# Performance work log

Measured on AMD Instinct MI355X. Metric: run time of the kernel, lower is better.

## Reference

```python
import jax, jax.numpy as jnp
import numpy as np

H = 8          # num_heads
DIM = 1024     # embed dim
DH = DIM // H // 2   # per-branch head dim = 64
B, N = 2, 2048
LAMBDA_INIT = 0.5
COS_MIN, COS_MAX = 0.0, 15.0
ALPHA = 0.5            # cos_head_residual_alpha
COS_EPS = 1e-6
RMS_EPS = 1e-5
# raw init so that sigmoid(raw) = (cos_scale_init - min)/(max - min) = 1/15
RAW_INIT = float(np.log((1.0/15.0) / (1.0 - 1.0/15.0)))


def setup_inputs() -> dict:
    key = jax.random.key(0)
    ks = jax.random.split(key, 10)
    s = 1.0 / np.sqrt(DIM)
    return {
        "x": jax.random.normal(ks[0], (B, N, DIM), jnp.float32),
        "Wq": jax.random.normal(ks[1], (DIM, DIM), jnp.float32) * s,
        "Wk": jax.random.normal(ks[2], (DIM, DIM), jnp.float32) * s,
        "Wv": jax.random.normal(ks[3], (DIM, DIM), jnp.float32) * s,
        "Wo": jax.random.normal(ks[4], (DIM, DIM), jnp.float32) * s,
        "bo": jnp.zeros((DIM,), jnp.float32),
        "lambda_q1": jax.random.normal(ks[5], (DH,), jnp.float32) * 0.1,
        "lambda_k1": jax.random.normal(ks[6], (DH,), jnp.float32) * 0.1,
        "lambda_q2": jax.random.normal(ks[7], (DH,), jnp.float32) * 0.1,
        "lambda_k2": jax.random.normal(ks[8], (DH,), jnp.float32) * 0.1,
        "delta_gain": jax.random.normal(ks[9], (H,), jnp.float32) * 0.1,
        "cos_head_delta": jnp.zeros((H,), jnp.float32),
        "cos_logit_scale_raw": jnp.float32(RAW_INIT),
        "subln_weight": jnp.ones((2 * DH,), jnp.float32),
    }


def _l2norm(t):
    # F.normalize: x / max(||x||_2, eps)
    return t / jnp.maximum(jnp.linalg.norm(t, axis=-1, keepdims=True), COS_EPS)


def reference(x, Wq, Wk, Wv, Wo, bo,
              lambda_q1, lambda_k1, lambda_q2, lambda_k2,
              delta_gain, cos_head_delta, cos_logit_scale_raw, subln_weight):
    b, n, c = x.shape
    # projections (torch Linear: x @ W.T)
    q = (x @ Wq.T).reshape(b, n, H, 2, DH).transpose(0, 2, 3, 1, 4)  # (B,H,2,N,Dh)
    k = (x @ Wk.T).reshape(b, n, H, 2, DH).transpose(0, 2, 3, 1, 4)
    v = (x @ Wv.T).reshape(b, n, H, 2 * DH).transpose(0, 2, 1, 3)    # (B,H,N,2Dh)
    q1, q2 = q[:, :, 0], q[:, :, 1]
    k1, k2 = k[:, :, 0], k[:, :, 1]

    # smooth-bounded cosine logit scale with per-head residual
    gscale = COS_MIN + (COS_MAX - COS_MIN) * jax.nn.sigmoid(cos_logit_scale_raw)
    head_delta = cos_head_delta - cos_head_delta.mean()
    cos_scale = (gscale * (1.0 + ALPHA * jnp.tanh(head_delta))).reshape(1, H, 1, 1)

    L1 = jnp.einsum('bhnd,bhmd->bhnm', _l2norm(q1), _l2norm(k1)) * cos_scale
    L2 = jnp.einsum('bhnd,bhmd->bhnm', _l2norm(q2), _l2norm(k2)) * cos_scale
    L1 = jnp.nan_to_num(L1)
    L2 = jnp.nan_to_num(L2)

    # tanh-gated interaction between branches
    G = jnp.tanh(delta_gain.reshape(1, H, 1, 1) * (L1 - L2))
    A1 = jax.nn.softmax((L1 + G).astype(jnp.float32), axis=-1).astype(x.dtype)
    A2 = jax.nn.softmax((L2 - G).astype(jnp.float32), axis=-1).astype(x.dtype)

    lambda_1 = jnp.exp(jnp.sum(lambda_q1 * lambda_k1))
    lambda_2 = jnp.exp(jnp.sum(lambda_q2 * lambda_k2))
    lambda_full = (lambda_1 - lambda_2 + LAMBDA_INIT).astype(x.dtype)

    attn = A1 - lambda_full * A2
    y = jnp.einsum('bhnm,bhmd->bhnd', attn, v)  # (B,H,N,2Dh)

    # sub-layer RMSNorm over last dim (2*Dh) with affine weight
    y = y * jax.lax.rsqrt(jnp.mean(y * y, axis=-1, keepdims=True) + RMS_EPS) * subln_weight
    y = y * (1.0 - LAMBDA_INIT)

    y = y.transpose(0, 2, 1, 3).reshape(b, n, c)
    return y @ Wo.T + bo
```

## Files before the change

kernel.cpp:

```cpp
#include <hip/hip_runtime.h>
#include <hip/hip_bf16.h>
#include <cstdint>

typedef __attribute__((ext_vector_type(8))) short short8_t;
typedef __attribute__((ext_vector_type(4))) float f32x4;
typedef __attribute__((ext_vector_type(16))) float f32x16;

#define LOG2E 1.4426950408889634f

__device__ __forceinline__ ushort f2bf(float f){
  union { float f; uint32_t i; } x; x.f = f;
  uint32_t r = x.i + 0x7FFFu + ((x.i >> 16) & 1u);
  return (ushort)(r >> 16);
}
__device__ __forceinline__ float fexp2(float x){
  float r; asm("v_exp_f32 %0, %1" : "=v"(r) : "v"(x)); return r;
}
__device__ __forceinline__ uint32_t cvtpk_bf16(float lo, float hi){
  uint32_t r;
  asm("v_cvt_pk_bf16_f32 %0, %1, %2" : "=v"(r) : "v"(lo), "v"(hi));
  return r;
}
__device__ __forceinline__ void pl32swap(uint32_t &a, uint32_t &b){
  asm volatile("v_permlane32_swap_b32 %0, %1" : "+v"(a), "+v"(b));
}
union PF { uint32_t u[4]; short8_t v; };

__global__ __launch_bounds__(256) void cvt_all_kernel(const float* __restrict__ x,
                                                      const float* __restrict__ Wq,
                                                      const float* __restrict__ Wk,
                                                      const float* __restrict__ Wv,
                                                      const float* __restrict__ Wo,
                                                      ushort* __restrict__ xb,
                                                      ushort* __restrict__ wqb,
                                                      ushort* __restrict__ wkb,
                                                      ushort* __restrict__ wvb,
                                                      ushort* __restrict__ wob){
  int bid = blockIdx.x;
  const float* s; ushort* d; int i;
  if (bid < 4096){ s = x; d = xb; i = bid * 256 + threadIdx.x; }
  else {
    int sel = (bid - 4096) >> 10;
    s = sel == 0 ? Wq : sel == 1 ? Wk : sel == 2 ? Wv : Wo;
    d = sel == 0 ? wqb : sel == 1 ? wkb : sel == 2 ? wvb : wob;
    i = ((bid - 4096) & 1023) * 256 + threadIdx.x;
  }
  float4 v = ((const float4*)s)[i];
  ushort4 o;
  o.x = f2bf(v.x); o.y = f2bf(v.y); o.z = f2bf(v.z); o.w = f2bf(v.w);
  ((ushort4*)d)[i] = o;
}

__global__ void prep_kernel(const float* __restrict__ lq1, const float* __restrict__ lk1,
                            const float* __restrict__ lq2, const float* __restrict__ lk2,
                            const float* __restrict__ dgain, const float* __restrict__ chd,
                            const float* __restrict__ rawp, float* __restrict__ sc){
  int lane = threadIdx.x;
  float p1 = lq1[lane] * lk1[lane];
  float p2 = lq2[lane] * lk2[lane];
  #pragma unroll
  for (int o = 1; o < 64; o <<= 1){
    p1 += __shfl_xor(p1, o, 64);
    p2 += __shfl_xor(p2, o, 64);
  }
  if (lane == 0) sc[24] = expf(p1) - expf(p2) + 0.5f;
  if (lane < 8){
    float m = 0.f;
    for (int i = 0; i < 8; i++) m += chd[i];
    m *= 0.125f;
    float gs = 15.f / (1.f + expf(-rawp[0]));
    float cs = gs * (1.f + 0.5f * tanhf(chd[lane] - m));
    sc[lane]      = LOG2E * cs;
    sc[8 + lane]  = LOG2E * (cs + 1.f);
    sc[16 + lane] = 2.f * dgain[lane];
  }
}

__global__ __launch_bounds__(256) void gemm_qkv(const ushort* __restrict__ A,
                                                const ushort* __restrict__ wqb,
                                                const ushort* __restrict__ wkb,
                                                const ushort* __restrict__ wvb,
                                                ushort* __restrict__ Qs,
                                                ushort* __restrict__ Kn,
                                                ushort* __restrict__ Vt,
                                                const float* __restrict__ sc){
  constexpr int N = 1024, K = 1024;
  __shared__ ushort As[128*32];
  __shared__ ushort Bs[128*32];
  const int z = blockIdx.z;
  const ushort* Bm = z == 0 ? wqb : (z == 1 ? wkb : wvb);
  const int t = threadIdx.x;
  const int lane = t & 63;
  const int w = t >> 6;
  const int wr = w >> 1, wc = w & 1;
  const long Ar0 = (long)blockIdx.x * 128;
  const long Br0 = (long)blockIdx.y * 128;
  const int r15 = lane & 15;
  const int kb = (lane >> 4) * 8;

  f32x4 acc[4][4];
  #pragma unroll
  for (int m = 0; m < 4; m++)
    #pragma unroll
    for (int n = 0; n < 4; n++) acc[m][n] = (f32x4){0.f, 0.f, 0.f, 0.f};

  for (int k0 = 0; k0 < K; k0 += 32){
    __syncthreads();
    #pragma unroll
    for (int r = 0; r < 2; r++){
      int li = r * 256 + t;
      int row = li >> 2;
      int col = (li & 3) * 8;
      __builtin_amdgcn_global_load_lds(
        (const __attribute__((address_space(1))) uint32_t*)(A + (Ar0 + row) * K + k0 + col),
        (__attribute__((address_space(3))) uint32_t*)(As + li * 8), 16, 0, 0);
      __builtin_amdgcn_global_load_lds(
        (const __attribute__((address_space(1))) uint32_t*)(Bm + (Br0 + row) * K + k0 + col),
        (__attribute__((address_space(3))) uint32_t*)(Bs + li * 8), 16, 0, 0);
    }
    __syncthreads();
    short8_t af[4], bfv[4];
    #pragma unroll
    for (int m = 0; m < 4; m++) af[m]  = *(const short8_t*)(As + (wr*64 + m*16 + r15)*32 + kb);
    #pragma unroll
    for (int n = 0; n < 4; n++) bfv[n] = *(const short8_t*)(Bs + (wc*64 + n*16 + r15)*32 + kb);
    #pragma unroll
    for (int m = 0; m < 4; m++)
      #pragma unroll
      for (int n = 0; n < 4; n++)
        acc[m][n] = __builtin_amdgcn_mfma_f32_16x16x32_bf16(af[m], bfv[n], acc[m][n], 0, 0, 0);
  }

  const int fr = (lane >> 4) * 4;
  if (z == 2){
    #pragma unroll
    for (int m = 0; m < 4; m++){
      #pragma unroll
      for (int n = 0; n < 4; n++){
        long row0 = Ar0 + wr*64 + m*16 + fr;
        long col  = Br0 + wc*64 + n*16 + r15;
        int bidx = (int)(row0 >> 11);
        int tok  = (int)(row0 & 2047);
        int hh   = (int)(col >> 7);
        int dd   = (int)(col & 127);
        ushort4 pk;
        pk.x = f2bf(acc[m][n][0]); pk.y = f2bf(acc[m][n][1]);
        pk.z = f2bf(acc[m][n][2]); pk.w = f2bf(acc[m][n][3]);
        *(ushort4*)(Vt + ((long)((bidx*8 + hh)*128 + dd))*2048 + tok) = pk;
      }
    }
  } else {
    ushort* dst = (z == 0) ? Qs : Kn;
    const float qsc = (z == 0) ? sc[Br0 >> 7] : 1.f;
    #pragma unroll
    for (int m = 0; m < 4; m++){
      float ss[4] = {0.f, 0.f, 0.f, 0.f};
      #pragma unroll
      for (int n = 0; n < 4; n++)
        #pragma unroll
        for (int r = 0; r < 4; r++) ss[r] = fmaf(acc[m][n][r], acc[m][n][r], ss[r]);
      #pragma unroll
      for (int r = 0; r < 4; r++){
        ss[r] += __shfl_xor(ss[r], 1, 16);
        ss[r] += __shfl_xor(ss[r], 2, 16);
        ss[r] += __shfl_xor(ss[r], 4, 16);
        ss[r] += __shfl_xor(ss[r], 8, 16);
        ss[r] = qsc / fmaxf(sqrtf(ss[r]), 1e-6f);
      }
      long row0 = Ar0 + wr*64 + m*16 + fr;
      #pragma unroll
      for (int n = 0; n < 4; n++){
        long col = Br0 + wc*64 + n*16 + r15;
        #pragma unroll
        for (int r = 0; r < 4; r++)
          dst[(row0 + r) * N + col] = f2bf(acc[m][n][r] * ss[r]);
      }
    }
  }
}

__global__ __launch_bounds__(256) void gemm_o64(const ushort* __restrict__ A,
                                                const ushort* __restrict__ Bm,
                                                float* __restrict__ Cout,
                                                const float* __restrict__ bias){
  constexpr int N = 1024, K = 1024;
  __shared__ ushort As[64*32];
  __shared__ ushort Bs[128*32];
  const int t = threadIdx.x;
  const int lane = t & 63;
  const int w = t >> 6;
  const int wr = w >> 1, wc = w & 1;
  const long Ar0 = (long)blockIdx.x * 64;
  const long Br0 = (long)blockIdx.y * 128;
  const int r15 = lane & 15;
  const int kb = (lane >> 4) * 8;

  f32x4 acc[2][4];
  #pragma unroll
  for (int m = 0; m < 2; m++)
    #pragma unroll
    for (int n = 0; n < 4; n++) acc[m][n] = (f32x4){0.f, 0.f, 0.f, 0.f};

  for (int k0 = 0; k0 < K; k0 += 32){
    __syncthreads();
    #pragma unroll
    for (int r = 0; r < 3; r++){
      int li = r * 256 + t;
      if (li < 256){
        int row = li >> 2;
        int col = (li & 3) * 8;
        __builtin_amdgcn_global_load_lds(
          (const __attribute__((address_space(1))) uint32_t*)(A + (Ar0 + row) * K + k0 + col),
          (__attribute__((address_space(3))) uint32_t*)(As + li * 8), 16, 0, 0);
      } else {
        int bi = li - 256;
        int row = bi >> 2;
        int col = (bi & 3) * 8;
        __builtin_amdgcn_global_load_lds(
          (const __attribute__((address_space(1))) uint32_t*)(Bm + (Br0 + row) * K + k0 + col),
          (__attribute__((address_space(3))) uint32_t*)(Bs + bi * 8), 16, 0, 0);
      }
    }
    __syncthreads();
    short8_t af[2], bfv[4];
    #pragma unroll
    for (int m = 0; m < 2; m++) af[m]  = *(const short8_t*)(As + (wr*32 + m*16 + r15)*32 + kb);
    #pragma unroll
    for (int n = 0; n < 4; n++) bfv[n] = *(const short8_t*)(Bs + (wc*64 + n*16 + r15)*32 + kb);
    #pragma unroll
    for (int m = 0; m < 2; m++)
      #pragma unroll
      for (int n = 0; n < 4; n++)
        acc[m][n] = __builtin_amdgcn_mfma_f32_16x16x32_bf16(af[m], bfv[n], acc[m][n], 0, 0, 0);
  }

  const int fr = (lane >> 4) * 4;
  #pragma unroll
  for (int m = 0; m < 2; m++){
    #pragma unroll
    for (int n = 0; n < 4; n++){
      long row0 = Ar0 + wr*32 + m*16 + fr;
      long col  = Br0 + wc*64 + n*16 + r15;
      float bsv = bias[col];
      #pragma unroll
      for (int r = 0; r < 4; r++)
        Cout[(row0 + r) * N + col] = acc[m][n][r] + bsv;
    }
  }
}

__global__ __launch_bounds__(256, 2) void attn6_kernel(
    const ushort* __restrict__ Qs, const ushort* __restrict__ Kn,
    const ushort* __restrict__ Vt, ushort* __restrict__ Yb,
    const float* __restrict__ sc, const float* __restrict__ subw){
  __shared__ ushort KV[2][2][8192];
  __shared__ float Zb[2][2][64];
  const int t = threadIdx.x;
  const int w = t >> 6;
  const int l = t & 63;
  const int lo5 = l & 31;
  const int hi = l >> 5;
  const int qt = w >> 1;
  const int kp = w & 1;
  const int bh = blockIdx.y;
  const int b = bh >> 3, h = bh & 7;
  const int q0 = blockIdx.x * 64 + qt * 32;
  const float dgh2 = sc[16 + h];
  const float lam  = sc[24];
  const int f2 = (lo5 & 3) ^ ((lo5 >> 2) & 3);

  short8_t qf[8];
  {
    const ushort* qp = Qs + (long)(b*2048 + q0 + lo5) * 1024 + h*128 + hi*8;
    #pragma unroll
    for (int c = 0; c < 2; c++)
      #pragma unroll
      for (int kc = 0; kc < 4; kc++)
        qf[c*4 + kc] = *(const short8_t*)(qp + c*64 + kc*16);
  }

  f32x16 y1a[4], y2a[4];
  #pragma unroll
  for (int nt = 0; nt < 4; nt++)
    #pragma unroll
    for (int i = 0; i < 16; i++){ y1a[nt][i] = 0.f; y2a[nt][i] = 0.f; }
  float Z1 = 0.f, Z2 = 0.f;

  const long kslice = (long)b * 2048 * 1024 + h * 128;
  const long vslice = (long)(b*8 + h) * 128 * 2048;

  int koff[2], kdst[2], voff[2], vdst[2];
  #pragma unroll
  for (int r = 0; r < 2; r++){
    int c = r * 256 + t;
    int key = c >> 4, ci = c & 15;
    kdst[r] = c * 8;
    koff[r] = key * 1024 + ((ci ^ (key & 15)) * 8);
    int dim = c >> 2, ci2 = c & 3;
    int fv = (dim & 3) ^ ((dim >> 2) & 3);
    vdst[r] = 4096 + c * 8;
    voff[r] = dim * 2048 + ((ci2 ^ fv) * 8);
  }

  auto stage = [&](int tileKp, int buf, int ktAbs){
    const ushort* bk = Kn + kslice + (long)ktAbs * 1024;
    const ushort* bv = Vt + vslice + ktAbs;
    ushort* dst = &KV[tileKp][buf][0];
    #pragma unroll
    for (int r = 0; r < 2; r++){
      __builtin_amdgcn_global_load_lds(
        (const __attribute__((address_space(1))) uint32_t*)(bk + koff[r]),
        (__attribute__((address_space(3))) uint32_t*)(dst + kdst[r]), 16, 0, 0);
      __builtin_amdgcn_global_load_lds(
        (const __attribute__((address_space(1))) uint32_t*)(bv + voff[r]),
        (__attribute__((address_space(3))) uint32_t*)(dst + vdst[r]), 16, 0, 0);
    }
  };

  stage(0, 0, 0);
  stage(1, 0, 1024);
  int buf = 0;
  for (int it = 0; it < 32; it++, buf ^= 1){
    __syncthreads();
    if (it + 1 < 32){
      stage(0, buf ^ 1, (it + 1) * 32);
      stage(1, buf ^ 1, 1024 + (it + 1) * 32);
    }
    const ushort* Ks = &KV[kp][buf][0];
    const ushort* Vs = &KV[kp][buf][4096];

    const int key = lo5;
    const int krow = key * 128;
    const int ksw = key & 15;
    f32x16 s1, s2;
    #pragma unroll
    for (int i = 0; i < 16; i++){ s1[i] = 0.f; s2[i] = 0.f; }
    #pragma unroll
    for (int kc = 0; kc < 4; kc++){
      short8_t kf = *(const short8_t*)(Ks + krow + (((kc*2 + hi) ^ ksw) * 8));
      s1 = __builtin_amdgcn_mfma_f32_32x32x16_bf16(kf, qf[kc], s1, 0, 0, 0);
    }
    #pragma unroll
    for (int kc = 0; kc < 4; kc++){
      short8_t kf = *(const short8_t*)(Ks + krow + (((8 + kc*2 + hi) ^ ksw) * 8));
      s2 = __builtin_amdgcn_mfma_f32_32x32x16_bf16(kf, qf[4 + kc], s2, 0, 0, 0);
    }

    uint32_t pa1[8], pa2[8];
    #pragma unroll
    for (int ks = 0; ks < 2; ks++){
      #pragma unroll
      for (int u = 0; u < 2; u++){
        const int rr = 8*ks + 2*u;
        float e1[4], e2[4];
        #pragma unroll
        for (int g4 = 0; g4 < 4; g4++){
          const int r = rr + (g4 >> 1)*4 + (g4 & 1);
          float a = s1[r], c = s2[r];
          float e  = fexp2(dgh2 * (a - c));
          float rc = __builtin_amdgcn_rcpf(e + 1.f);
          float gl = fmaf(-2.f * LOG2E, rc, LOG2E);
          float p1 = fexp2(a + gl);
          float p2 = fexp2(c - gl);
          Z1 += p1; Z2 += p2;
          e1[g4] = p1; e2[g4] = p2;
        }
        uint32_t a1 = cvtpk_bf16(e1[0], e1[1]), b1 = cvtpk_bf16(e1[2], e1[3]);
        uint32_t a2 = cvtpk_bf16(e2[0], e2[1]), b2 = cvtpk_bf16(e2[2], e2[3]);
        pl32swap(a1, b1);
        pl32swap(a2, b2);
        pa1[ks*4 + u] = a1; pa1[ks*4 + 2 + u] = b1;
        pa2[ks*4 + u] = a2; pa2[ks*4 + 2 + u] = b2;
      }
    }

    #pragma unroll
    for (int ks = 0; ks < 2; ks++){
      PF pf1, pf2;
      #pragma unroll
      for (int i = 0; i < 4; i++){ pf1.u[i] = pa1[ks*4 + i]; pf2.u[i] = pa2[ks*4 + i]; }
      const int ck = ks*2 + hi;
      #pragma unroll
      for (int nt = 0; nt < 4; nt++){
        const int dim = nt*32 + lo5;
        short8_t vf = *(const short8_t*)(Vs + dim*32 + ((ck ^ f2) * 8));
        y1a[nt] = __builtin_amdgcn_mfma_f32_32x32x16_bf16(pf1.v, vf, y1a[nt], 0, 0, 0);
        y2a[nt] = __builtin_amdgcn_mfma_f32_32x32x16_bf16(pf2.v, vf, y2a[nt], 0, 0, 0);
      }
    }
  }

  Z1 += __shfl_xor(Z1, 32, 64);
  Z2 += __shfl_xor(Z2, 32, 64);

  __syncthreads();
  float* Mb = (float*)(&KV[0][0][0]);
  if (kp == 1){
    #pragma unroll
    for (int nt = 0; nt < 4; nt++)
      #pragma unroll
      for (int i = 0; i < 16; i++){
        Mb[(((qt*2 + 0)*4 + nt)*16 + i)*64 + l] = y1a[nt][i];
        Mb[(((qt*2 + 1)*4 + nt)*16 + i)*64 + l] = y2a[nt][i];
      }
    Zb[qt][0][l] = Z1; Zb[qt][1][l] = Z2;
  }
  __syncthreads();
  if (kp == 1) return;

  #pragma unroll
  for (int nt = 0; nt < 4; nt++)
    #pragma unroll
    for (int i = 0; i < 16; i++){
      y1a[nt][i] += Mb[(((qt*2 + 0)*4 + nt)*16 + i)*64 + l];
      y2a[nt][i] += Mb[(((qt*2 + 1)*4 + nt)*16 + i)*64 + l];
    }
  Z1 += Zb[qt][0][l];
  Z2 += Zb[qt][1][l];

  #pragma unroll
  for (int r = 0; r < 16; r++){
    const int qr = (r & 3) + 8*(r >> 2) + 4*hi;
    float z1r = __shfl(Z1, (l & 32) | qr, 64);
    float z2r = __shfl(Z2, (l & 32) | qr, 64);
    float inv1 = 1.f / z1r;
    float inv2 = lam / z2r;
    float yv[4]; float ssq = 0.f;
    #pragma unroll
    for (int nt = 0; nt < 4; nt++){
      yv[nt] = y1a[nt][r]*inv1 - y2a[nt][r]*inv2;
      ssq = fmaf(yv[nt], yv[nt], ssq);
    }
    ssq += __shfl_xor(ssq, 1, 64);
    ssq += __shfl_xor(ssq, 2, 64);
    ssq += __shfl_xor(ssq, 4, 64);
    ssq += __shfl_xor(ssq, 8, 64);
    ssq += __shfl_xor(ssq, 16, 64);
    float rms = rsqrtf(ssq * (1.f / 128.f) + 1e-5f);
    const long tok = (long)b*2048 + q0 + qr;
    ushort* op = Yb + tok*1024 + h*128;
    #pragma unroll
    for (int nt = 0; nt < 4; nt++){
      const int dim = nt*32 + lo5;
      op[dim] = f2bf(yv[nt] * rms * subw[dim] * 0.5f);
    }
  }
}

extern "C" void kernel_launch(void* const* d_in, const int* in_sizes, int n_in,
                              void* d_out, int out_size, void* d_ws, size_t ws_size,
                              hipStream_t stream) {
  const float* x   = (const float*)d_in[0];
  const float* Wq  = (const float*)d_in[1];
  const float* Wk  = (const float*)d_in[2];
  const float* Wv  = (const float*)d_in[3];
  const float* Wo  = (const float*)d_in[4];
  const float* bo  = (const float*)d_in[5];
  const float* lq1 = (const float*)d_in[6];
  const float* lk1 = (const float*)d_in[7];
  const float* lq2 = (const float*)d_in[8];
  const float* lk2 = (const float*)d_in[9];
  const float* dg  = (const float*)d_in[10];
  const float* chd = (const float*)d_in[11];
  const float* raw = (const float*)d_in[12];
  const float* subw= (const float*)d_in[13];
  float* out = (float*)d_out;

  char* ws = (char*)d_ws;
  const size_t MB = 1024 * 1024;
  ushort* xb  = (ushort*)(ws);
  ushort* wqb = (ushort*)(ws + 8 * MB);
  ushort* wkb = wqb + 1024 * 1024;
  ushort* wvb = wkb + 1024 * 1024;
  ushort* wob = wvb + 1024 * 1024;
  ushort* Qs  = (ushort*)(ws + 16 * MB);
  ushort* Kn  = Qs + 4 * 1024 * 1024;
  ushort* Vt  = Kn + 4 * 1024 * 1024;
  ushort* Yb  = Vt + 4 * 1024 * 1024;
  float*  sc  = (float*)(Yb + 4 * 1024 * 1024);

  cvt_all_kernel<<<8192, 256, 0, stream>>>(x, Wq, Wk, Wv, Wo, xb, wqb, wkb, wvb, wob);
  prep_kernel<<<1, 64, 0, stream>>>(lq1, lk1, lq2, lk2, dg, chd, raw, sc);

  gemm_qkv<<<dim3(32, 8, 3), 256, 0, stream>>>(xb, wqb, wkb, wvb, Qs, Kn, Vt, sc);

  attn6_kernel<<<dim3(32, 16), 256, 0, stream>>>(Qs, Kn, Vt, Yb, sc, subw);

  gemm_o64<<<dim3(64, 8), 256, 0, stream>>>(Yb, wob, out, bo);
}
```

Measured before the change: 162.4 us.

## Single-buffer K/V LDS tiles and split merge into two passes to halve shared memory

Removes double buffering of K/V tiles in LDS, so each iteration loads and then synchronizes before compute, halving the attention kernel's LDS footprint. The cross-wave merge of y1/y2 accumulators is split into two sequential passes through a smaller scratch region. The goal is likely higher occupancy from reduced LDS per block, at the cost of losing load/compute overlap and adding extra barriers.

```diff
diff --git a/kernel.cpp b/kernel.cpp
--- a/kernel.cpp
+++ b/kernel.cpp
@@ -249,11 +249,11 @@
   }
 }
 
-__global__ __launch_bounds__(256, 2) void attn6_kernel(
+__global__ __launch_bounds__(256, 2) void attn9_kernel(
     const ushort* __restrict__ Qs, const ushort* __restrict__ Kn,
     const ushort* __restrict__ Vt, ushort* __restrict__ Yb,
     const float* __restrict__ sc, const float* __restrict__ subw){
-  __shared__ ushort KV[2][2][8192];
+  __shared__ ushort KV[2][8192];
   __shared__ float Zb[2][2][64];
   const int t = threadIdx.x;
   const int w = t >> 6;
@@ -302,10 +302,10 @@
     voff[r] = dim * 2048 + ((ci2 ^ fv) * 8);
   }
 
-  auto stage = [&](int tileKp, int buf, int ktAbs){
+  auto stage = [&](int tileKp, int ktAbs){
     const ushort* bk = Kn + kslice + (long)ktAbs * 1024;
     const ushort* bv = Vt + vslice + ktAbs;
-    ushort* dst = &KV[tileKp][buf][0];
+    ushort* dst = &KV[tileKp][0];
     #pragma unroll
     for (int r = 0; r < 2; r++){
       __builtin_amdgcn_global_load_lds(
@@ -317,17 +317,13 @@
     }
   };
 
-  stage(0, 0, 0);
-  stage(1, 0, 1024);
-  int buf = 0;
-  for (int it = 0; it < 32; it++, buf ^= 1){
-    __syncthreads();
-    if (it + 1 < 32){
-      stage(0, buf ^ 1, (it + 1) * 32);
-      stage(1, buf ^ 1, 1024 + (it + 1) * 32);
-    }
-    const ushort* Ks = &KV[kp][buf][0];
-    const ushort* Vs = &KV[kp][buf][4096];
+  for (int it = 0; it < 32; it++){
+    __syncthreads();
+    stage(0, it * 32);
+    stage(1, 1024 + it * 32);
+    __syncthreads();
+    const ushort* Ks = &KV[kp][0];
+    const ushort* Vs = &KV[kp][4096];
 
     const int key = lo5;
     const int krow = key * 128;
@@ -393,30 +389,41 @@
   Z1 += __shfl_xor(Z1, 32, 64);
   Z2 += __shfl_xor(Z2, 32, 64);
 
+  float* Mb = (float*)(&KV[0][0]);
   __syncthreads();
-  float* Mb = (float*)(&KV[0][0][0]);
   if (kp == 1){
     #pragma unroll
     for (int nt = 0; nt < 4; nt++)
       #pragma unroll
-      for (int i = 0; i < 16; i++){
-        Mb[(((qt*2 + 0)*4 + nt)*16 + i)*64 + l] = y1a[nt][i];
-        Mb[(((qt*2 + 1)*4 + nt)*16 + i)*64 + l] = y2a[nt][i];
-      }
+      for (int i = 0; i < 16; i++)
+        Mb[((qt*4 + nt)*16 + i)*64 + l] = y1a[nt][i];
     Zb[qt][0][l] = Z1; Zb[qt][1][l] = Z2;
+  }
+  __syncthreads();
+  if (kp == 0){
+    #pragma unroll
+    for (int nt = 0; nt < 4; nt++)
+      #pragma unroll
+      for (int i = 0; i < 16; i++)
+        y1a[nt][i] += Mb[((qt*4 + nt)*16 + i)*64 + l];
+    Z1 += Zb[qt][0][l];
+    Z2 += Zb[qt][1][l];
+  }
+  __syncthreads();
+  if (kp == 1){
+    #pragma unroll
+    for (int nt = 0; nt < 4; nt++)
+      #pragma unroll
+      for (int i = 0; i < 16; i++)
+        Mb[((qt*4 + nt)*16 + i)*64 + l] = y2a[nt][i];
   }
   __syncthreads();
   if (kp == 1) return;
-
   #pragma unroll
   for (int nt = 0; nt < 4; nt++)
     #pragma unroll
-    for (int i = 0; i < 16; i++){
-      y1a[nt][i] += Mb[(((qt*2 + 0)*4 + nt)*16 + i)*64 + l];
-      y2a[nt][i] += Mb[(((qt*2 + 1)*4 + nt)*16 + i)*64 + l];
-    }
-  Z1 += Zb[qt][0][l];
-  Z2 += Zb[qt][1][l];
+    for (int i = 0; i < 16; i++)
+      y2a[nt][i] += Mb[((qt*4 + nt)*16 + i)*64 + l];
 
   #pragma unroll
   for (int r = 0; r < 16; r++){
@@ -484,7 +491,7 @@
 
   gemm_qkv<<<dim3(32, 8, 3), 256, 0, stream>>>(xb, wqb, wkb, wvb, Qs, Kn, Vt, sc);
 
-  attn6_kernel<<<dim3(32, 16), 256, 0, stream>>>(Qs, Kn, Vt, Yb, sc, subw);
+  attn9_kernel<<<dim3(32, 16), 256, 0, stream>>>(Qs, Kn, Vt, Yb, sc, subw);
 
   gemm_o64<<<dim3(64, 8), 256, 0, stream>>>(Yb, wob, out, bo);
 }
```

After: 162.2 us, median of 2. Within noise of the previous version (-0.1%).
